# Optimization experiments

Hardware: AMD Instinct MI355X
Metric: run time of the kernel (lower is better)

Reference implementation:

```python
import jax, jax.numpy as jnp
from jax import lax
import numpy as np

S, N, E = 4, 50000, 800000
D_IN, D_NOISE, D_H, D_OUT = 96, 32, 32, 128
F_CAT = D_IN + D_NOISE + D_H  # 160, matches nn.Linear(input_dim+noise_dim+32, out)


def setup_inputs() -> dict:
    key = jax.random.key(0)
    ks = jax.random.split(key, 8)
    X = jax.random.normal(ks[0], (1, N, D_IN), dtype=jnp.float32)
    h = jax.random.normal(ks[1], (1, N, D_H), dtype=jnp.float32)
    # Bernoulli(0.5) noise, sampled in setup for determinism (original samples in forward)
    epsilon = (jax.random.uniform(ks[2], (S, N, D_NOISE)) < 0.5).astype(jnp.float32)
    W = jax.random.normal(ks[3], (F_CAT, D_OUT), dtype=jnp.float32) * 0.02
    b = jnp.zeros((D_OUT,), dtype=jnp.float32)
    gin_eps = jnp.zeros((), dtype=jnp.float32)  # init_eps=0, learn_eps=True
    src = jax.random.randint(ks[4], (E,), 0, N, dtype=jnp.int32)
    dst = jax.random.randint(ks[5], (E,), 0, N, dtype=jnp.int32)
    return {"X": X, "h": h, "epsilon": epsilon, "W": W, "b": b,
            "gin_eps": gin_eps, "src": src, "dst": dst}


def reference(X, h, epsilon, W, b, gin_eps, src, dst):
    # X: [1,N,D_IN] expanded to sample_size; h: [1,N,32] expanded; epsilon: [S,N,D_NOISE]
    s, n = epsilon.shape[0], X.shape[1]
    Xb = jnp.broadcast_to(X, (s, n, X.shape[2]))
    hb = jnp.broadcast_to(h, (s, n, h.shape[2]))
    x_all = jnp.concatenate([Xb, epsilon, hb], axis=2)  # [S,N,F_CAT]

    def per_sample(carry, x):  # x: [N,F_CAT]
        # GINConv('sum'): (1+eps)*x + sum_{j in N(i)} x_j, then Linear, then activation
        agg = (1.0 + gin_eps) * x + jax.ops.segment_sum(x[src], dst, num_segments=n)
        y = jax.nn.relu(agg @ W + b)           # [N,D_OUT]
        return carry, jnp.mean(y, axis=0)      # per-layer mean over nodes -> [D_OUT]

    _, means = lax.scan(per_sample, None, x_all)  # [S,D_OUT]
    # outputTensor[i] = tempdim12 broadcasts the [D_OUT] vector over the node axis
    out = jnp.broadcast_to(means[:, None, :], (s, n, W.shape[1]))
    return jax.nn.relu(out), epsilon
```

## Files before the change

kernel.cpp:

```cpp
#include <hip/hip_runtime.h>

#define N_NODES  50000
#define N_EDGES  800000
#define D_OUTF   128
#define F_PACK   256
#define NTILES   3125
#define GEMM_BLOCKS 256
#define NB1      196
#define PBX 6250
#define PBB 25000
#define PBH 3125
#define PBW 80
#define PB_TOT (PBX + PBB + PBH + PBW + 1)

#define OUTB_F4  6400000
#define EPS_OFF  25600000L
#define INV_N    (1.0f / (float)N_NODES)

typedef __attribute__((ext_vector_type(8))) short bf16x8;
typedef __attribute__((ext_vector_type(4))) float f32x4;
typedef __attribute__((ext_vector_type(2))) float f32x2;

__device__ __forceinline__ unsigned short f2bf(float x) {
  unsigned int u = __float_as_uint(x);
  u += 0x7FFFu + ((u >> 16) & 1u);
  return (unsigned short)(u >> 16);
}
__device__ __forceinline__ unsigned int pack2(float a, float b) {
  return (unsigned int)f2bf(a) | ((unsigned int)f2bf(b) << 16);
}
__device__ __forceinline__ unsigned int spreadLo(unsigned int rep) {
  return (((rep & 0x08040201u) + 0x7F7F7F7Fu) >> 7) & 0x01010101u;
}
__device__ __forceinline__ unsigned int spreadHi(unsigned int rep) {
  return (((rep & 0x80402010u) + 0x7F7F7F7Fu) >> 7) & 0x01010101u;
}
__device__ __forceinline__ void f8acc(unsigned int w, float& a0, float& a1,
                                      float& a2, float& a3) {
  f32x2 p0 = __builtin_amdgcn_cvt_pk_f32_fp8(w, false);
  f32x2 p1 = __builtin_amdgcn_cvt_pk_f32_fp8(w, true);
  a0 += p0.x; a1 += p0.y; a2 += p1.x; a3 += p1.y;
}

__global__ void k_pack(const float* __restrict__ X, const float* __restrict__ h,
                       const float* __restrict__ eps, const float* __restrict__ W,
                       const int* __restrict__ dst,
                       unsigned int* __restrict__ featF8,
                       unsigned int* __restrict__ epsb, int* __restrict__ cnt,
                       unsigned short* __restrict__ Wp,
                       float* __restrict__ outEps, float* __restrict__ sums,
                       int* __restrict__ done) {
  int blk = blockIdx.x, tid = threadIdx.x;
  if (blk < PBX) {
    int t = blk * 256 + tid;
    int node = t >> 5, f = (t & 31) << 2;
    float a0, a1, a2, a3;
    if (f < 96) {
      const float* p = X + node * 96 + f;
      a0 = p[0]; a1 = p[1]; a2 = p[2]; a3 = p[3];
    } else {
      const float* p = h + node * 32 + (f - 96);
      a0 = p[0]; a1 = p[1]; a2 = p[2]; a3 = p[3];
    }
    unsigned int d = __builtin_amdgcn_cvt_pk_fp8_f32(a0, a1, 0, false);
    d = __builtin_amdgcn_cvt_pk_fp8_f32(a2, a3, d, true);
    featF8[t] = d;
  } else if (blk < PBX + PBB) {
    long g = (long)(blk - PBX) * 256 + tid;
    float v = eps[g];
    outEps[g] = v;
    unsigned long long m = __ballot(v > 0.5f);
    int lane = tid & 63;
    if ((lane & 31) == 0) {
      long idx = g >> 5;
      int s = (int)(idx / N_NODES);
      int node = (int)(idx - (long)s * N_NODES);
      epsb[node * 4 + s] = (unsigned int)(m >> ((lane >> 5) * 32));
    }
  } else if (blk < PBX + PBB + PBH) {
    int i = (blk - PBX - PBB) * 256 + tid;
    atomicAdd(&cnt[dst[i]], 1);
  } else if (blk < PBX + PBB + PBH + PBW) {
    int t = (blk - (PBX + PBB + PBH)) * 256 + tid;
    int j = t & 7, col = (t >> 3) & 15, quad = (t >> 7) & 3, r = t >> 9;
    int kb5 = r % 5, i2 = r / 5;
    int wr;
    if (kb5 < 4) {
      int k = kb5 * 32 + quad * 8 + j;
      wr = (k < 96) ? k : k + 32;
    } else {
      wr = 96 + quad * 8 + j;
    }
    Wp[t] = f2bf(W[wr * D_OUTF + i2 * 16 + col]);
  } else {
    sums[tid] = 0.f;
    sums[tid + 256] = 0.f;
    if (tid < 2) done[tid] = 0;
  }
}

__global__ void k_scan1(const int* __restrict__ cnt, int* __restrict__ excl,
                        int* __restrict__ bsum, int* __restrict__ boff,
                        int* __restrict__ done) {
  __shared__ int wpart[4];
  __shared__ int sd[256];
  __shared__ int lastf;
  int tid = threadIdx.x, lane = tid & 63, wid = tid >> 6;
  int i = blockIdx.x * 256 + tid;
  int v = (i < N_NODES) ? cnt[i] : 0;
  int x = v;
#pragma unroll
  for (int d = 1; d < 64; d <<= 1) {
    int t = __shfl_up(x, d, 64);
    if (lane >= d) x += t;
  }
  if (lane == 63) wpart[wid] = x;
  __syncthreads();
  if (tid == 0) {
    int s = 0;
#pragma unroll
    for (int w = 0; w < 4; ++w) { int t = wpart[w]; wpart[w] = s; s += t; }
    __hip_atomic_store(&bsum[blockIdx.x], s, __ATOMIC_RELEASE,
                       __HIP_MEMORY_SCOPE_AGENT);
    int d = __hip_atomic_fetch_add(done, 1, __ATOMIC_ACQ_REL,
                                   __HIP_MEMORY_SCOPE_AGENT);
    lastf = (d == NB1 - 1);
  }
  __syncthreads();
  if (i < N_NODES) excl[i] = wpart[wid] + x - v;
  if (lastf) {
    int bv = (tid < NB1)
                 ? __hip_atomic_load(&bsum[tid], __ATOMIC_ACQUIRE,
                                     __HIP_MEMORY_SCOPE_AGENT)
                 : 0;
    sd[tid] = bv;
    __syncthreads();
    for (int d = 1; d < 256; d <<= 1) {
      int t = (tid >= d) ? sd[tid - d] : 0;
      __syncthreads();
      sd[tid] += t;
      __syncthreads();
    }
    if (tid < NB1) boff[tid] = sd[tid] - bv;
  }
}

__global__ void k_scatter(const int* __restrict__ src, const int* __restrict__ dst,
                          const int* __restrict__ excl, const int* __restrict__ boff,
                          int* __restrict__ cnt, int* __restrict__ csr) {
  int i = blockIdx.x * blockDim.x + threadIdx.x;
  if (i < N_EDGES) {
    int d = dst[i];
    int r = atomicAdd(&cnt[d], -1);
    csr[excl[d] + boff[d >> 8] + r - 1] = src[i];
  }
}

__global__ __launch_bounds__(256) void k_agg_ep(
    const uint2* __restrict__ feat2, const unsigned int* __restrict__ epsw,
    const float* __restrict__ geps_p, const int* __restrict__ excl,
    const int* __restrict__ boff, const int* __restrict__ csr,
    uint4* __restrict__ agg4) {
  int wave = (blockIdx.x * blockDim.x + threadIdx.x) >> 6;
  int lane = threadIdx.x & 63;
  int li = lane & 15, es = lane >> 4;
  if (wave >= N_NODES) return;
  int n = wave;
  float ge = 1.0f + geps_p[0];
  int wsel = li >> 2, bsh = (li & 3) * 8;

  int off_n = excl[n] + boff[n >> 8];
  int e1 = (n == N_NODES - 1) ? N_EDGES : excl[n + 1] + boff[(n + 1) >> 8];

  uint2 sf = feat2[n * 16 + li];
  unsigned int swd = epsw[n * 4 + wsel];

  float af0 = 0.f, af1 = 0.f, af2 = 0.f, af3 = 0.f;
  float af4 = 0.f, af5 = 0.f, af6 = 0.f, af7 = 0.f;
  unsigned int accLo = 0, accHi = 0;

  int e = off_n + es;
  for (; e + 4 < e1; e += 8) {
    int s0 = csr[e], s1 = csr[e + 4];
    uint2 f0 = feat2[s0 * 16 + li];
    uint2 f1 = feat2[s1 * 16 + li];
    unsigned int w0 = epsw[s0 * 4 + wsel];
    unsigned int w1 = epsw[s1 * 4 + wsel];
    f8acc(f0.x, af0, af1, af2, af3);  f8acc(f0.y, af4, af5, af6, af7);
    f8acc(f1.x, af0, af1, af2, af3);  f8acc(f1.y, af4, af5, af6, af7);
    unsigned int B0 = (w0 >> bsh) & 0xFFu;
    unsigned int B1 = (w1 >> bsh) & 0xFFu;
    unsigned int r0 = B0 | (B0 << 8);  r0 |= r0 << 16;
    unsigned int r1 = B1 | (B1 << 8);  r1 |= r1 << 16;
    accLo += spreadLo(r0) + spreadLo(r1);
    accHi += spreadHi(r0) + spreadHi(r1);
  }
  if (e < e1) {
    int s0 = csr[e];
    uint2 f0 = feat2[s0 * 16 + li];
    unsigned int w0 = epsw[s0 * 4 + wsel];
    f8acc(f0.x, af0, af1, af2, af3);  f8acc(f0.y, af4, af5, af6, af7);
    unsigned int B0 = (w0 >> bsh) & 0xFFu;
    unsigned int r0 = B0 | (B0 << 8);  r0 |= r0 << 16;
    accLo += spreadLo(r0);
    accHi += spreadHi(r0);
  }

#pragma unroll
  for (int d = 16; d < 64; d <<= 1) {
    af0 += __shfl_xor(af0, d, 64);  af1 += __shfl_xor(af1, d, 64);
    af2 += __shfl_xor(af2, d, 64);  af3 += __shfl_xor(af3, d, 64);
    af4 += __shfl_xor(af4, d, 64);  af5 += __shfl_xor(af5, d, 64);
    af6 += __shfl_xor(af6, d, 64);  af7 += __shfl_xor(af7, d, 64);
    accLo += __shfl_xor((int)accLo, d, 64);
    accHi += __shfl_xor((int)accHi, d, 64);
  }

  if (es == 0) {
    f32x2 s0 = __builtin_amdgcn_cvt_pk_f32_fp8(sf.x, false);
    f32x2 s1 = __builtin_amdgcn_cvt_pk_f32_fp8(sf.x, true);
    f32x2 s2 = __builtin_amdgcn_cvt_pk_f32_fp8(sf.y, false);
    f32x2 s3 = __builtin_amdgcn_cvt_pk_f32_fp8(sf.y, true);
    af0 += ge * s0.x;  af1 += ge * s0.y;
    af2 += ge * s1.x;  af3 += ge * s1.y;
    af4 += ge * s2.x;  af5 += ge * s2.y;
    af6 += ge * s3.x;  af7 += ge * s3.y;
    unsigned int Bself = (swd >> bsh) & 0xFFu;
    float ev0 = ge * (float)(Bself & 1u)        + (float)(accLo & 0xFFu);
    float ev1 = ge * (float)((Bself >> 1) & 1u) + (float)((accLo >> 8) & 0xFFu);
    float ev2 = ge * (float)((Bself >> 2) & 1u) + (float)((accLo >> 16) & 0xFFu);
    float ev3 = ge * (float)((Bself >> 3) & 1u) + (float)((accLo >> 24) & 0xFFu);
    float ev4 = ge * (float)((Bself >> 4) & 1u) + (float)(accHi & 0xFFu);
    float ev5 = ge * (float)((Bself >> 5) & 1u) + (float)((accHi >> 8) & 0xFFu);
    float ev6 = ge * (float)((Bself >> 6) & 1u) + (float)((accHi >> 16) & 0xFFu);
    float ev7 = ge * (float)((Bself >> 7) & 1u) + (float)((accHi >> 24) & 0xFFu);

    uint4 oXh, oEp;
    oXh.x = pack2(af0, af1); oXh.y = pack2(af2, af3);
    oXh.z = pack2(af4, af5); oXh.w = pack2(af6, af7);
    oEp.x = pack2(ev0, ev1); oEp.y = pack2(ev2, ev3);
    oEp.z = pack2(ev4, ev5); oEp.w = pack2(ev6, ev7);
    agg4[n * 32 + li]      = oXh;
    agg4[n * 32 + 16 + li] = oEp;
  }
}

__global__ __launch_bounds__(512) void k_gemm(const uint4* __restrict__ agg4,
    const unsigned short* __restrict__ Wp, const float* __restrict__ b,
    float* __restrict__ sums) {
  __shared__ uint4 lds[2][544];
  int tid = threadIdx.x;
  int lane = tid & 63;
  int w = tid >> 6;
  int col = lane & 15;
  int quad = lane >> 4;

  const bf16x8* wp8 = (const bf16x8*)Wp;
  bf16x8 Bsh[4], Bep;
  float bias = b[w * 16 + col];
#pragma unroll
  for (int kb = 0; kb < 4; ++kb)
    Bsh[kb] = wp8[((w * 5 + kb) * 4 + quad) * 16 + col];
  Bep = wp8[((w * 5 + 4) * 4 + quad) * 16 + col];

  int p1 = tid, row1 = p1 / 33, c1 = p1 - row1 * 33;
  int p2 = 512 + tid, row2 = p2 / 33, c2 = p2 - row2 * 33;
  bool v1 = (c1 < 32);
  bool v2 = (tid < 16) && (c2 < 32);

  f32x4 psum[4];
#pragma unroll
  for (int s = 0; s < 4; ++s) psum[s] = (f32x4){0.f, 0.f, 0.f, 0.f};

  {
    int t0 = blockIdx.x;
    if (v1) lds[0][p1] = agg4[t0 * 512 + row1 * 32 + c1];
    if (v2) lds[0][p2] = agg4[t0 * 512 + row2 * 32 + c2];
  }
  int cur = 0;
  for (int t = blockIdx.x; t < NTILES; t += GEMM_BLOCKS) {
    int t2 = t + GEMM_BLOCKS;
    if (t2 >= NTILES) t2 = t;
    uint4 r1, r2;
    if (v1) r1 = agg4[t2 * 512 + row1 * 32 + c1];
    if (v2) r2 = agg4[t2 * 512 + row2 * 32 + c2];

    __syncthreads();

    const uint4* base = &lds[cur][col * 33];
    bf16x8 Ash[4];
#pragma unroll
    for (int kb = 0; kb < 4; ++kb)
      Ash[kb] = *(const bf16x8*)(base + kb * 4 + quad);
    f32x4 csh = (f32x4){0.f, 0.f, 0.f, 0.f};
#pragma unroll
    for (int kb = 0; kb < 4; ++kb)
      csh = __builtin_amdgcn_mfma_f32_16x16x32_bf16(Ash[kb], Bsh[kb], csh, 0, 0, 0);
#pragma unroll
    for (int s = 0; s < 4; ++s) {
      bf16x8 Aep = *(const bf16x8*)(base + 16 + s * 4 + quad);
      f32x4 c = __builtin_amdgcn_mfma_f32_16x16x32_bf16(Aep, Bep, csh, 0, 0, 0);
#pragma unroll
      for (int r = 0; r < 4; ++r)
        psum[s][r] += fmaxf(c[r] + bias, 0.f);
    }

    if (v1) lds[cur ^ 1][p1] = r1;
    if (v2) lds[cur ^ 1][p2] = r2;
    cur ^= 1;
  }

#pragma unroll
  for (int s = 0; s < 4; ++s) {
    float v = psum[s][0] + psum[s][1] + psum[s][2] + psum[s][3];
    v += __shfl_xor(v, 16, 64);
    v += __shfl_xor(v, 32, 64);
    if (quad == 0)
      atomicAdd(&sums[s * 128 + w * 16 + col], v);
  }
}

__global__ void k_out(const float* __restrict__ sums, float* __restrict__ out) {
  int i = blockIdx.x * 256 + threadIdx.x;
  int o4 = i & 31;
  unsigned int sn = (unsigned int)i >> 5;
  unsigned int s = sn / (unsigned int)N_NODES;
  float4 sv = ((const float4*)sums)[s * 32 + o4];
  float4 ov;
  ov.x = fmaxf(sv.x * INV_N, 0.f);
  ov.y = fmaxf(sv.y * INV_N, 0.f);
  ov.z = fmaxf(sv.z * INV_N, 0.f);
  ov.w = fmaxf(sv.w * INV_N, 0.f);
  ((float4*)out)[i] = ov;
}

extern "C" void kernel_launch(void* const* d_in, const int* in_sizes, int n_in,
                              void* d_out, int out_size, void* d_ws, size_t ws_size,
                              hipStream_t stream) {
  const float* X    = (const float*)d_in[0];
  const float* h    = (const float*)d_in[1];
  const float* eps  = (const float*)d_in[2];
  const float* W    = (const float*)d_in[3];
  const float* b    = (const float*)d_in[4];
  const float* geps = (const float*)d_in[5];
  const int*   src  = (const int*)d_in[6];
  const int*   dst  = (const int*)d_in[7];
  float* out = (float*)d_out;

  char* w = (char*)d_ws;
  unsigned int*  featF8 = (unsigned int*)w;  w += (size_t)N_NODES * 32 * 4;
  unsigned int*  epsb   = (unsigned int*)w;  w += (size_t)N_NODES * 4 * 4;
  unsigned int*  agg_u  = (unsigned int*)w;  w += (size_t)N_NODES * 128 * 4;
  int*   excl     = (int*)w;   w += (size_t)(N_NODES + 16) * 4;
  int*   cnt      = (int*)w;   w += (size_t)N_NODES * 4;
  int*   csr      = (int*)w;   w += (size_t)N_EDGES * 4;
  int*   bsum     = (int*)w;   w += 256 * 4;
  int*   boff     = (int*)w;   w += 256 * 4;
  unsigned short* Wp = (unsigned short*)w; w += (size_t)20480 * 2;
  float* sums     = (float*)w; w += 512 * 4;
  int*   done     = (int*)w;   w += 64;

  int eb = (N_EDGES + 255) / 256;
  hipMemsetAsync(cnt, 0, (size_t)N_NODES * 4, stream);
  k_pack<<<PB_TOT, 256, 0, stream>>>(X, h, eps, W, dst, featF8, epsb, cnt, Wp,
                                     out + EPS_OFF, sums, done);
  k_scan1<<<NB1, 256, 0, stream>>>(cnt, excl, bsum, boff, &done[0]);
  k_scatter<<<eb, 256, 0, stream>>>(src, dst, excl, boff, cnt, csr);

  k_agg_ep<<<(N_NODES * 64) / 256, 256, 0, stream>>>((const uint2*)featF8, epsb,
                                                     geps, excl, boff, csr,
                                                     (uint4*)agg_u);

  k_gemm<<<GEMM_BLOCKS, 512, 0, stream>>>((const uint4*)agg_u, Wp, b, sums);

  k_out<<<OUTB_F4 / 256, 256, 0, stream>>>(sums, out);
}
```

Baseline: 319.4 us.

## Fuse neighbor aggregation into GEMM kernel via LDS, replicate partial sums

Merges the gather-aggregate kernel and the MFMA GEMM kernel into one persistent kernel. Each block aggregates 16 nodes directly into a double-buffered LDS tile and runs the MFMA on it, so the bf16 aggregate buffer (N×256 bytes) is never written to or read back from global memory. The final per-column atomic sums are spread over 8 replicas to reduce atomic contention, and k_out adds the replicas back together. The tradeoff is that the latency-bound gather can no longer overlap with GEMM loads across kernels, and each block is serialized by a barrier per tile. Occupancy may also drop at 512 threads with the added register use.

```diff
diff --git a/kernel.cpp b/kernel.cpp
--- a/kernel.cpp
+++ b/kernel.cpp
@@ -5,7 +5,8 @@
 #define D_OUTF   128
 #define F_PACK   256
 #define NTILES   3125
-#define GEMM_BLOCKS 256
+#define GRID_AG  1024
+#define R_SUM    8
 #define NB1      196
 #define PBX 6250
 #define PBB 25000
@@ -48,7 +49,7 @@
                        unsigned int* __restrict__ featF8,
                        unsigned int* __restrict__ epsb, int* __restrict__ cnt,
                        unsigned short* __restrict__ Wp,
-                       float* __restrict__ outEps, float* __restrict__ sums,
+                       float* __restrict__ outEps, float* __restrict__ sums2,
                        int* __restrict__ done) {
   int blk = blockIdx.x, tid = threadIdx.x;
   if (blk < PBX) {
@@ -93,8 +94,9 @@
     }
     Wp[t] = f2bf(W[wr * D_OUTF + i2 * 16 + col]);
   } else {
-    sums[tid] = 0.f;
-    sums[tid + 256] = 0.f;
+#pragma unroll
+    for (int r = 0; r < (R_SUM * 512) / 256; ++r)
+      sums2[r * 256 + tid] = 0.f;
     if (tid < 2) done[tid] = 0;
   }
 }
@@ -156,138 +158,119 @@
   }
 }
 
-__global__ __launch_bounds__(256) void k_agg_ep(
+__global__ __launch_bounds__(512) void k_aggemm(
     const uint2* __restrict__ feat2, const unsigned int* __restrict__ epsw,
     const float* __restrict__ geps_p, const int* __restrict__ excl,
     const int* __restrict__ boff, const int* __restrict__ csr,
-    uint4* __restrict__ agg4) {
-  int wave = (blockIdx.x * blockDim.x + threadIdx.x) >> 6;
-  int lane = threadIdx.x & 63;
+    const unsigned short* __restrict__ Wp, const float* __restrict__ bias_p,
+    float* __restrict__ sums2) {
+  __shared__ uint4 lds[2][16][33];
+  int tid = threadIdx.x;
+  int lane = tid & 63;
+  int wv = tid >> 6;
   int li = lane & 15, es = lane >> 4;
-  if (wave >= N_NODES) return;
-  int n = wave;
+  int col = li, quad = es;
   float ge = 1.0f + geps_p[0];
   int wsel = li >> 2, bsh = (li & 3) * 8;
 
-  int off_n = excl[n] + boff[n >> 8];
-  int e1 = (n == N_NODES - 1) ? N_EDGES : excl[n + 1] + boff[(n + 1) >> 8];
-
-  uint2 sf = feat2[n * 16 + li];
-  unsigned int swd = epsw[n * 4 + wsel];
-
-  float af0 = 0.f, af1 = 0.f, af2 = 0.f, af3 = 0.f;
-  float af4 = 0.f, af5 = 0.f, af6 = 0.f, af7 = 0.f;
-  unsigned int accLo = 0, accHi = 0;
-
-  int e = off_n + es;
-  for (; e + 4 < e1; e += 8) {
-    int s0 = csr[e], s1 = csr[e + 4];
-    uint2 f0 = feat2[s0 * 16 + li];
-    uint2 f1 = feat2[s1 * 16 + li];
-    unsigned int w0 = epsw[s0 * 4 + wsel];
-    unsigned int w1 = epsw[s1 * 4 + wsel];
-    f8acc(f0.x, af0, af1, af2, af3);  f8acc(f0.y, af4, af5, af6, af7);
-    f8acc(f1.x, af0, af1, af2, af3);  f8acc(f1.y, af4, af5, af6, af7);
-    unsigned int B0 = (w0 >> bsh) & 0xFFu;
-    unsigned int B1 = (w1 >> bsh) & 0xFFu;
-    unsigned int r0 = B0 | (B0 << 8);  r0 |= r0 << 16;
-    unsigned int r1 = B1 | (B1 << 8);  r1 |= r1 << 16;
-    accLo += spreadLo(r0) + spreadLo(r1);
-    accHi += spreadHi(r0) + spreadHi(r1);
-  }
-  if (e < e1) {
-    int s0 = csr[e];
-    uint2 f0 = feat2[s0 * 16 + li];
-    unsigned int w0 = epsw[s0 * 4 + wsel];
-    f8acc(f0.x, af0, af1, af2, af3);  f8acc(f0.y, af4, af5, af6, af7);
-    unsigned int B0 = (w0 >> bsh) & 0xFFu;
-    unsigned int r0 = B0 | (B0 << 8);  r0 |= r0 << 16;
-    accLo += spreadLo(r0);
-    accHi += spreadHi(r0);
-  }
-
-#pragma unroll
-  for (int d = 16; d < 64; d <<= 1) {
-    af0 += __shfl_xor(af0, d, 64);  af1 += __shfl_xor(af1, d, 64);
-    af2 += __shfl_xor(af2, d, 64);  af3 += __shfl_xor(af3, d, 64);
-    af4 += __shfl_xor(af4, d, 64);  af5 += __shfl_xor(af5, d, 64);
-    af6 += __shfl_xor(af6, d, 64);  af7 += __shfl_xor(af7, d, 64);
-    accLo += __shfl_xor((int)accLo, d, 64);
-    accHi += __shfl_xor((int)accHi, d, 64);
-  }
-
-  if (es == 0) {
-    f32x2 s0 = __builtin_amdgcn_cvt_pk_f32_fp8(sf.x, false);
-    f32x2 s1 = __builtin_amdgcn_cvt_pk_f32_fp8(sf.x, true);
-    f32x2 s2 = __builtin_amdgcn_cvt_pk_f32_fp8(sf.y, false);
-    f32x2 s3 = __builtin_amdgcn_cvt_pk_f32_fp8(sf.y, true);
-    af0 += ge * s0.x;  af1 += ge * s0.y;
-    af2 += ge * s1.x;  af3 += ge * s1.y;
-    af4 += ge * s2.x;  af5 += ge * s2.y;
-    af6 += ge * s3.x;  af7 += ge * s3.y;
-    unsigned int Bself = (swd >> bsh) & 0xFFu;
-    float ev0 = ge * (float)(Bself & 1u)        + (float)(accLo & 0xFFu);
-    float ev1 = ge * (float)((Bself >> 1) & 1u) + (float)((accLo >> 8) & 0xFFu);
-    float ev2 = ge * (float)((Bself >> 2) & 1u) + (float)((accLo >> 16) & 0xFFu);
-    float ev3 = ge * (float)((Bself >> 3) & 1u) + (float)((accLo >> 24) & 0xFFu);
-    float ev4 = ge * (float)((Bself >> 4) & 1u) + (float)(accHi & 0xFFu);
-    float ev5 = ge * (float)((Bself >> 5) & 1u) + (float)((accHi >> 8) & 0xFFu);
-    float ev6 = ge * (float)((Bself >> 6) & 1u) + (float)((accHi >> 16) & 0xFFu);
-    float ev7 = ge * (float)((Bself >> 7) & 1u) + (float)((accHi >> 24) & 0xFFu);
-
-    uint4 oXh, oEp;
-    oXh.x = pack2(af0, af1); oXh.y = pack2(af2, af3);
-    oXh.z = pack2(af4, af5); oXh.w = pack2(af6, af7);
-    oEp.x = pack2(ev0, ev1); oEp.y = pack2(ev2, ev3);
-    oEp.z = pack2(ev4, ev5); oEp.w = pack2(ev6, ev7);
-    agg4[n * 32 + li]      = oXh;
-    agg4[n * 32 + 16 + li] = oEp;
-  }
-}
-
-__global__ __launch_bounds__(512) void k_gemm(const uint4* __restrict__ agg4,
-    const unsigned short* __restrict__ Wp, const float* __restrict__ b,
-    float* __restrict__ sums) {
-  __shared__ uint4 lds[2][544];
-  int tid = threadIdx.x;
-  int lane = tid & 63;
-  int w = tid >> 6;
-  int col = lane & 15;
-  int quad = lane >> 4;
-
   const bf16x8* wp8 = (const bf16x8*)Wp;
   bf16x8 Bsh[4], Bep;
-  float bias = b[w * 16 + col];
+  float bias = bias_p[wv * 16 + col];
 #pragma unroll
   for (int kb = 0; kb < 4; ++kb)
-    Bsh[kb] = wp8[((w * 5 + kb) * 4 + quad) * 16 + col];
-  Bep = wp8[((w * 5 + 4) * 4 + quad) * 16 + col];
-
-  int p1 = tid, row1 = p1 / 33, c1 = p1 - row1 * 33;
-  int p2 = 512 + tid, row2 = p2 / 33, c2 = p2 - row2 * 33;
-  bool v1 = (c1 < 32);
-  bool v2 = (tid < 16) && (c2 < 32);
+    Bsh[kb] = wp8[((wv * 5 + kb) * 4 + quad) * 16 + col];
+  Bep = wp8[((wv * 5 + 4) * 4 + quad) * 16 + col];
 
   f32x4 psum[4];
 #pragma unroll
   for (int s = 0; s < 4; ++s) psum[s] = (f32x4){0.f, 0.f, 0.f, 0.f};
 
-  {
-    int t0 = blockIdx.x;
-    if (v1) lds[0][p1] = agg4[t0 * 512 + row1 * 32 + c1];
-    if (v2) lds[0][p2] = agg4[t0 * 512 + row2 * 32 + c2];
-  }
-  int cur = 0;
-  for (int t = blockIdx.x; t < NTILES; t += GEMM_BLOCKS) {
-    int t2 = t + GEMM_BLOCKS;
-    if (t2 >= NTILES) t2 = t;
-    uint4 r1, r2;
-    if (v1) r1 = agg4[t2 * 512 + row1 * 32 + c1];
-    if (v2) r2 = agg4[t2 * 512 + row2 * 32 + c2];
+  int buf = 0;
+  for (int t = blockIdx.x; t < NTILES; t += GRID_AG) {
+#pragma unroll
+    for (int p = 0; p < 2; ++p) {
+      int n = t * 16 + p * 8 + wv;
+
+      int off_n = excl[n] + boff[n >> 8];
+      int e1 = (n == N_NODES - 1) ? N_EDGES : excl[n + 1] + boff[(n + 1) >> 8];
+
+      uint2 sf = feat2[n * 16 + li];
+      unsigned int swd = epsw[n * 4 + wsel];
+
+      float af0 = 0.f, af1 = 0.f, af2 = 0.f, af3 = 0.f;
+      float af4 = 0.f, af5 = 0.f, af6 = 0.f, af7 = 0.f;
+      unsigned int accLo = 0, accHi = 0;
+
+      int e = off_n + es;
+      for (; e + 4 < e1; e += 8) {
+        int s0 = csr[e], s1 = csr[e + 4];
+        uint2 f0 = feat2[s0 * 16 + li];
+        uint2 f1 = feat2[s1 * 16 + li];
+        unsigned int w0 = epsw[s0 * 4 + wsel];
+        unsigned int w1 = epsw[s1 * 4 + wsel];
+        f8acc(f0.x, af0, af1, af2, af3);  f8acc(f0.y, af4, af5, af6, af7);
+        f8acc(f1.x, af0, af1, af2, af3);  f8acc(f1.y, af4, af5, af6, af7);
+        unsigned int B0 = (w0 >> bsh) & 0xFFu;
+        unsigned int B1 = (w1 >> bsh) & 0xFFu;
+        unsigned int r0 = B0 | (B0 << 8);  r0 |= r0 << 16;
+        unsigned int r1 = B1 | (B1 << 8);  r1 |= r1 << 16;
+        accLo += spreadLo(r0) + spreadLo(r1);
+        accHi += spreadHi(r0) + spreadHi(r1);
+      }
+      if (e < e1) {
+        int s0 = csr[e];
+        uint2 f0 = feat2[s0 * 16 + li];
+        unsigned int w0 = epsw[s0 * 4 + wsel];
+        f8acc(f0.x, af0, af1, af2, af3);  f8acc(f0.y, af4, af5, af6, af7);
+        unsigned int B0 = (w0 >> bsh) & 0xFFu;
+        unsigned int r0 = B0 | (B0 << 8);  r0 |= r0 << 16;
+        accLo += spreadLo(r0);
+        accHi += spreadHi(r0);
+      }
+
+#pragma unroll
+      for (int d = 16; d < 64; d <<= 1) {
+        af0 += __shfl_xor(af0, d, 64);  af1 += __shfl_xor(af1, d, 64);
+        af2 += __shfl_xor(af2, d, 64);  af3 += __shfl_xor(af3, d, 64);
+        af4 += __shfl_xor(af4, d, 64);  af5 += __shfl_xor(af5, d, 64);
+        af6 += __shfl_xor(af6, d, 64);  af7 += __shfl_xor(af7, d, 64);
+        accLo += __shfl_xor((int)accLo, d, 64);
+        accHi += __shfl_xor((int)accHi, d, 64);
+      }
+
+      if (es == 0) {
+        f32x2 s0 = __builtin_amdgcn_cvt_pk_f32_fp8(sf.x, false);
+        f32x2 s1 = __builtin_amdgcn_cvt_pk_f32_fp8(sf.x, true);
+        f32x2 s2 = __builtin_amdgcn_cvt_pk_f32_fp8(sf.y, false);
+        f32x2 s3 = __builtin_amdgcn_cvt_pk_f32_fp8(sf.y, true);
+        af0 += ge * s0.x;  af1 += ge * s0.y;
+        af2 += ge * s1.x;  af3 += ge * s1.y;
+        af4 += ge * s2.x;  af5 += ge * s2.y;
+        af6 += ge * s3.x;  af7 += ge * s3.y;
+        unsigned int Bself = (swd >> bsh) & 0xFFu;
+        float ev0 = ge * (float)(Bself & 1u)        + (float)(accLo & 0xFFu);
+        float ev1 = ge * (float)((Bself >> 1) & 1u) + (float)((accLo >> 8) & 0xFFu);
+        float ev2 = ge * (float)((Bself >> 2) & 1u) + (float)((accLo >> 16) & 0xFFu);
+        float ev3 = ge * (float)((Bself >> 3) & 1u) + (float)((accLo >> 24) & 0xFFu);
+        float ev4 = ge * (float)((Bself >> 4) & 1u) + (float)(accHi & 0xFFu);
+        float ev5 = ge * (float)((Bself >> 5) & 1u) + (float)((accHi >> 8) & 0xFFu);
+        float ev6 = ge * (float)((Bself >> 6) & 1u) + (float)((accHi >> 16) & 0xFFu);
+        float ev7 = ge * (float)((Bself >> 7) & 1u) + (float)((accHi >> 24) & 0xFFu);
+
+        uint4 oXh, oEp;
+        oXh.x = pack2(af0, af1); oXh.y = pack2(af2, af3);
+        oXh.z = pack2(af4, af5); oXh.w = pack2(af6, af7);
+        oEp.x = pack2(ev0, ev1); oEp.y = pack2(ev2, ev3);
+        oEp.z = pack2(ev4, ev5); oEp.w = pack2(ev6, ev7);
+        int j = p * 8 + wv;
+        lds[buf][j][li]      = oXh;
+        lds[buf][j][16 + li] = oEp;
+      }
+    }
 
     __syncthreads();
 
-    const uint4* base = &lds[cur][col * 33];
+    const uint4* base = &lds[buf][col][0];
     bf16x8 Ash[4];
 #pragma unroll
     for (int kb = 0; kb < 4; ++kb)
@@ -305,32 +288,37 @@
         psum[s][r] += fmaxf(c[r] + bias, 0.f);
     }
 
-    if (v1) lds[cur ^ 1][p1] = r1;
-    if (v2) lds[cur ^ 1][p2] = r2;
-    cur ^= 1;
-  }
-
+    buf ^= 1;
+  }
+
+  int rep = blockIdx.x & (R_SUM - 1);
 #pragma unroll
   for (int s = 0; s < 4; ++s) {
     float v = psum[s][0] + psum[s][1] + psum[s][2] + psum[s][3];
     v += __shfl_xor(v, 16, 64);
     v += __shfl_xor(v, 32, 64);
     if (quad == 0)
-      atomicAdd(&sums[s * 128 + w * 16 + col], v);
-  }
-}
-
-__global__ void k_out(const float* __restrict__ sums, float* __restrict__ out) {
+      atomicAdd(&sums2[rep * 512 + s * 128 + wv * 16 + col], v);
+  }
+}
+
+__global__ void k_out(const float* __restrict__ sums2, float* __restrict__ out) {
   int i = blockIdx.x * 256 + threadIdx.x;
   int o4 = i & 31;
   unsigned int sn = (unsigned int)i >> 5;
   unsigned int s = sn / (unsigned int)N_NODES;
-  float4 sv = ((const float4*)sums)[s * 32 + o4];
+  const float4* sp = (const float4*)sums2;
+  float4 a = {0.f, 0.f, 0.f, 0.f};
+#pragma unroll
+  for (int r = 0; r < R_SUM; ++r) {
+    float4 t = sp[r * 128 + s * 32 + o4];
+    a.x += t.x; a.y += t.y; a.z += t.z; a.w += t.w;
+  }
   float4 ov;
-  ov.x = fmaxf(sv.x * INV_N, 0.f);
-  ov.y = fmaxf(sv.y * INV_N, 0.f);
-  ov.z = fmaxf(sv.z * INV_N, 0.f);
-  ov.w = fmaxf(sv.w * INV_N, 0.f);
+  ov.x = fmaxf(a.x * INV_N, 0.f);
+  ov.y = fmaxf(a.y * INV_N, 0.f);
+  ov.z = fmaxf(a.z * INV_N, 0.f);
+  ov.w = fmaxf(a.w * INV_N, 0.f);
   ((float4*)out)[i] = ov;
 }
 
@@ -350,28 +338,24 @@
   char* w = (char*)d_ws;
   unsigned int*  featF8 = (unsigned int*)w;  w += (size_t)N_NODES * 32 * 4;
   unsigned int*  epsb   = (unsigned int*)w;  w += (size_t)N_NODES * 4 * 4;
-  unsigned int*  agg_u  = (unsigned int*)w;  w += (size_t)N_NODES * 128 * 4;
   int*   excl     = (int*)w;   w += (size_t)(N_NODES + 16) * 4;
   int*   cnt      = (int*)w;   w += (size_t)N_NODES * 4;
   int*   csr      = (int*)w;   w += (size_t)N_EDGES * 4;
   int*   bsum     = (int*)w;   w += 256 * 4;
   int*   boff     = (int*)w;   w += 256 * 4;
   unsigned short* Wp = (unsigned short*)w; w += (size_t)20480 * 2;
-  float* sums     = (float*)w; w += 512 * 4;
+  float* sums2    = (float*)w; w += (size_t)R_SUM * 512 * 4;
   int*   done     = (int*)w;   w += 64;
 
   int eb = (N_EDGES + 255) / 256;
   hipMemsetAsync(cnt, 0, (size_t)N_NODES * 4, stream);
   k_pack<<<PB_TOT, 256, 0, stream>>>(X, h, eps, W, dst, featF8, epsb, cnt, Wp,
-                                     out + EPS_OFF, sums, done);
+                                     out + EPS_OFF, sums2, done);
   k_scan1<<<NB1, 256, 0, stream>>>(cnt, excl, bsum, boff, &done[0]);
   k_scatter<<<eb, 256, 0, stream>>>(src, dst, excl, boff, cnt, csr);
 
-  k_agg_ep<<<(N_NODES * 64) / 256, 256, 0, stream>>>((const uint2*)featF8, epsb,
-                                                     geps, excl, boff, csr,
-                                                     (uint4*)agg_u);
-
-  k_gemm<<<GEMM_BLOCKS, 512, 0, stream>>>((const uint4*)agg_u, Wp, b, sums);
-
-  k_out<<<OUTB_F4 / 256, 256, 0, stream>>>(sums, out);
-}
+  k_aggemm<<<GRID_AG, 512, 0, stream>>>((const uint2*)featF8, epsb, geps,
+                                        excl, boff, csr, Wp, b, sums2);
+
+  k_out<<<OUTB_F4 / 256, 256, 0, stream>>>(sums2, out);
+}
```

After: 342.1 us. 1.07x slower.
